# Optimization experiments

Measured on AMD Instinct MI355X. Metric: run time of the kernel, lower is better.

The kernel has to match this reference:

```python
import jax, jax.numpy as jnp
import numpy as np
import math

DEPTH = 3
RATIO = 0.5
EPS = 1e-5


def _mlp_ln(h, W1, b1, W2, b2, W3, b3, g, beta):
    h = jax.nn.gelu(h @ W1 + b1, approximate=False)
    h = jax.nn.gelu(h @ W2 + b2, approximate=False)
    h = h @ W3 + b3
    mu = jnp.mean(h, axis=-1, keepdims=True)
    var = jnp.mean((h - mu) ** 2, axis=-1, keepdims=True)
    return g * (h - mu) * jax.lax.rsqrt(var + EPS) + beta


def _node_to_node(x, s, r, n, p):
    # two-way gather -> scatter_add -> MLP+LN. Row n of x_pad is a zero dummy
    # node that absorbs edges dropped by pooling (fixed-size, jit-friendly).
    x_pad = jnp.concatenate([x, jnp.zeros((1, x.shape[1]), x.dtype)], axis=0)
    msg = x_pad[jnp.concatenate([s, r])]            # [2E, C]
    recv = jnp.concatenate([r, s])                  # [2E]
    agg = jax.ops.segment_sum(msg, recv, num_segments=n + 1)[:n]
    return _mlp_ln(agg, *p)


def _forward(x, senders, receivers, pool_w, down_p, up_p):
    s, r = senders, receivers
    xs, edges, perms = [x], [(s, r)], []
    n = x.shape[0]
    for i in range(DEPTH):
        k = math.ceil(RATIO * n)  # PyG topk: ceil(ratio * N)
        w = pool_w[i]
        score = jnp.tanh(x @ w / jnp.linalg.norm(w))
        vals, perm = jax.lax.top_k(score, k)
        x = x[perm] * vals[:, None]
        # remap edges; dropped nodes (and old dummy n) map to new dummy k
        nmap = jnp.full((n + 1,), k, dtype=s.dtype).at[perm].set(
            jnp.arange(k, dtype=s.dtype))
        ns_, nr_ = nmap[s], nmap[r]
        invalid = (ns_ == k) | (nr_ == k)
        s = jnp.where(invalid, k, ns_)
        r = jnp.where(invalid, k, nr_)
        x = _node_to_node(x, s, r, k, down_p[i])
        if i < DEPTH - 1:
            xs.append(x)
            edges.append((s, r))
        perms.append(perm)
        n = k
    for i in range(DEPTH):
        j = DEPTH - 1 - i
        res = xs[j]
        s, r = edges[j]
        perm = perms[j]
        up = jnp.zeros_like(res).at[perm].set(x)
        x = jnp.concatenate([res, up], axis=-1)  # sum_res=False -> concat
        x = _node_to_node(x, s, r, res.shape[0], up_p[i])
    return x


def setup_inputs() -> dict:
    key = jax.random.key(0)
    ks = jax.random.split(key, 16)
    N, E, C, D = 50000, 600000, 128, DEPTH
    f32 = jnp.float32

    def lin(k, fi, fo):
        return (jax.random.normal(k, (D, fi, fo), f32) / np.sqrt(fi)).astype(f32)

    return {
        'x': jax.random.normal(ks[0], (N, C), f32),
        'senders': jax.random.randint(ks[1], (E,), 0, N, dtype=jnp.int32),
        'receivers': jax.random.randint(ks[2], (E,), 0, N, dtype=jnp.int32),
        'pool_w': jax.random.normal(ks[3], (D, C), f32),
        'down_W1': lin(ks[4], C, C), 'down_b1': jnp.zeros((D, C), f32),
        'down_W2': lin(ks[5], C, C), 'down_b2': jnp.zeros((D, C), f32),
        'down_W3': lin(ks[6], C, C), 'down_b3': jnp.zeros((D, C), f32),
        'down_g': jnp.ones((D, C), f32), 'down_beta': jnp.zeros((D, C), f32),
        'up_W1': lin(ks[7], 2 * C, C), 'up_b1': jnp.zeros((D, C), f32),
        'up_W2': lin(ks[8], C, C), 'up_b2': jnp.zeros((D, C), f32),
        'up_W3': lin(ks[9], C, C), 'up_b3': jnp.zeros((D, C), f32),
        'up_g': jnp.ones((D, C), f32), 'up_beta': jnp.zeros((D, C), f32),
    }


def reference(x, senders, receivers, pool_w,
              down_W1, down_b1, down_W2, down_b2, down_W3, down_b3,
              down_g, down_beta,
              up_W1, up_b1, up_W2, up_b2, up_W3, up_b3, up_g, up_beta):
    down_p = [(down_W1[i], down_b1[i], down_W2[i], down_b2[i],
               down_W3[i], down_b3[i], down_g[i], down_beta[i])
              for i in range(DEPTH)]
    up_p = [(up_W1[i], up_b1[i], up_W2[i], up_b2[i],
             up_W3[i], up_b3[i], up_g[i], up_beta[i])
            for i in range(DEPTH)]
    return _forward(x, senders, receivers, pool_w, down_p, up_p)
```

## Files before the change

### kernel.cpp

```cpp
#include <hip/hip_runtime.h>
#include <math.h>


typedef unsigned short u16;
typedef short bf16x8 __attribute__((ext_vector_type(8)));
typedef float f32x4 __attribute__((ext_vector_type(4)));

__device__ __forceinline__ unsigned int fkey(float f) {
  unsigned int b = __float_as_uint(f);
  return (b & 0x80000000u) ? ~b : (b | 0x80000000u);
}

__device__ __forceinline__ float gelu_f(float v) {
  return 0.5f * v * (1.0f + erff(v * 0.70710678118654752f));
}

__device__ __forceinline__ u16 f2bf(float f) {
  unsigned u = __float_as_uint(f);
  u = (u + 0x7FFFu + ((u >> 16) & 1u)) >> 16;
  return (u16)u;
}
__device__ __forceinline__ float bf2f(u16 u) {
  return __uint_as_float(((unsigned)u) << 16);
}

__global__ void score_kernel(const float* __restrict__ x, const float* __restrict__ w,
                             float* __restrict__ key, float* __restrict__ valt, int n) {
  int wave = threadIdx.x >> 6, lane = threadIdx.x & 63;
  int i = blockIdx.x * 4 + wave;
  if (i >= n) return;
  float2 xv = *(const float2*)&x[(size_t)i * 128 + lane * 2];
  float2 wv = *(const float2*)&w[lane * 2];
  double d  = (double)xv.x * wv.x + (double)xv.y * wv.y;
  double nw = (double)wv.x * wv.x + (double)wv.y * wv.y;
  for (int o = 32; o; o >>= 1) { d += __shfl_down(d, o, 64); nw += __shfl_down(nw, o, 64); }
  if (lane == 0) {
    key[i]  = (float)d;
    valt[i] = (float)tanh(d / sqrt(nw));
  }
}

__global__ void preamble_kernel(const float* __restrict__ x, u16* __restrict__ xb, int n,
                                const float* __restrict__ uW1, const float* __restrict__ uW2,
                                const float* __restrict__ uW3, u16* __restrict__ wt1,
                                u16* __restrict__ wt2, u16* __restrict__ wt3,
                                const float* __restrict__ poolw, double* __restrict__ sqn,
                                u16* __restrict__ z0, u16* __restrict__ z1,
                                u16* __restrict__ z2, int nbX) {
  int b = blockIdx.x;
  if (b < nbX) {
    int gid = b * 256 + threadIdx.x;
    if (gid < n * 32) {
      float4 a = *(const float4*)&x[(size_t)gid * 4];
      *(ushort4*)&xb[(size_t)gid * 4] =
          make_ushort4(f2bf(a.x), f2bf(a.y), f2bf(a.z), f2bf(a.w));
    }
    return;
  }
  b -= nbX;
  if (b < 768) {
    int i = b * 256 + threadIdx.x;
    int lvl = i >> 16, rem = i & 65535;
    if (rem < 32768) {
      int k = rem >> 7, c = rem & 127;
      wt1[(size_t)lvl * 32768 + c * 256 + k] = f2bf(uW1[(size_t)lvl * 32768 + rem]);
    } else if (rem < 49152) {
      int j = rem - 32768; int k = j >> 7, c = j & 127;
      wt2[(size_t)lvl * 16384 + c * 128 + k] = f2bf(uW2[(size_t)lvl * 16384 + j]);
    } else {
      int j = rem - 49152; int k = j >> 7, c = j & 127;
      wt3[(size_t)lvl * 16384 + c * 128 + k] = f2bf(uW3[(size_t)lvl * 16384 + j]);
    }
    return;
  }
  b -= 768;
  if (b == 0) {
    if (threadIdx.x < 64) {
      int lane = threadIdx.x;
      for (int l = 0; l < 3; ++l) {
        float2 wv = *(const float2*)&poolw[l * 128 + lane * 2];
        double nw = (double)wv.x * wv.x + (double)wv.y * wv.y;
        for (int o = 32; o; o >>= 1) nw += __shfl_down(nw, o, 64);
        if (lane == 0) sqn[l] = sqrt(nw);
      }
    }
    return;
  }
  int t = threadIdx.x;
  if (t < 128) { z0[t] = 0; z1[t] = 0; z2[t] = 0; }
}

__global__ void hist_hi_kernel(const float* __restrict__ key, int* __restrict__ hist,
                               int* __restrict__ csum, int n) {
  __shared__ int lc[256];
  lc[threadIdx.x] = 0;
  __syncthreads();
  int i = blockIdx.x * 256 + threadIdx.x;
  if (i < n) {
    unsigned b = fkey(key[i]) >> 16;
    atomicAdd(&hist[b], 1);
    atomicAdd(&lc[b >> 8], 1);
  }
  __syncthreads();
  int v = lc[threadIdx.x];
  if (v) atomicAdd(&csum[threadIdx.x], v);
}

__global__ void hist_lo_kernel(const float* __restrict__ key, const int* __restrict__ meta,
                               int* __restrict__ hist, int* __restrict__ csum, int n) {
  __shared__ int lc[256];
  lc[threadIdx.x] = 0;
  __syncthreads();
  int i = blockIdx.x * 256 + threadIdx.x;
  if (i < n) {
    unsigned u = fkey(key[i]);
    if ((u >> 16) == (unsigned)meta[0]) {
      unsigned b = u & 0xFFFFu;
      atomicAdd(&hist[b], 1);
      atomicAdd(&lc[b >> 8], 1);
    }
  }
  __syncthreads();
  int v = lc[threadIdx.x];
  if (v) atomicAdd(&csum[threadIdx.x], v);
}

__global__ void find_hi2_kernel(const int* __restrict__ hist, const int* __restrict__ csum,
                                int* __restrict__ meta, int k) {
  __shared__ int s[256];
  __shared__ int cSh, cumSh;
  int t = threadIdx.x;
  s[t] = csum[t];
  __syncthreads();
  if (t == 0) {
    int cum = 0, c = 0;
    for (int i = 255; i >= 0; --i) {
      if (cum + s[i] >= k) { c = i; break; }
      cum += s[i];
    }
    cSh = c; cumSh = cum;
  }
  __syncthreads();
  int c = cSh;
  s[t] = hist[c * 256 + t];
  __syncthreads();
  if (t == 0) {
    int cum = cumSh;
    for (int b = 255; b >= 0; --b) {
      int v = s[b];
      if (cum + v >= k) { meta[0] = c * 256 + b; meta[1] = k - cum; break; }
      cum += v;
    }
  }
}

__global__ void find_lo2_kernel(const int* __restrict__ hist, const int* __restrict__ csum,
                                int* __restrict__ meta) {
  __shared__ int s[256];
  __shared__ int cSh, cumSh;
  int t = threadIdx.x;
  int m = meta[1], B = meta[0];
  s[t] = csum[t];
  __syncthreads();
  if (t == 0) {
    int cum = 0, c = 0;
    for (int i = 255; i >= 0; --i) {
      if (cum + s[i] >= m) { c = i; break; }
      cum += s[i];
    }
    cSh = c; cumSh = cum;
  }
  __syncthreads();
  int c = cSh;
  s[t] = hist[c * 256 + t];
  __syncthreads();
  if (t == 0) {
    int cum = cumSh;
    for (int b = 255; b >= 0; --b) {
      int v = s[b];
      if (cum + v >= m) {
        meta[3] = (int)((((unsigned)B) << 16) | (unsigned)(c * 256 + b));
        meta[4] = m - cum;
        break;
      }
      cum += v;
    }
    meta[5] = 0;
  }
}

__global__ void tie_count_kernel(const float* __restrict__ key, const int* __restrict__ meta,
                                 int* __restrict__ tcnt, int n) {
  __shared__ int cnt[4];
  unsigned uT = (unsigned)meta[3];
  int i = blockIdx.x * 256 + threadIdx.x;
  bool tie = (i < n) && (fkey(key[i]) == uT);
  unsigned long long m = __ballot(tie);
  int lane = threadIdx.x & 63, w = threadIdx.x >> 6;
  if (lane == 0) cnt[w] = __popcll(m);
  __syncthreads();
  if (threadIdx.x == 0) tcnt[blockIdx.x] = cnt[0] + cnt[1] + cnt[2] + cnt[3];
}

__global__ void tie_mark_kernel(const float* __restrict__ key, const int* __restrict__ meta,
                                const int* __restrict__ tcnt, unsigned char* __restrict__ selt,
                                int n) {
  __shared__ int red[256];
  __shared__ int woff[4];
  int t = threadIdx.x;
  red[t] = (t < (int)blockIdx.x) ? tcnt[t] : 0;
  __syncthreads();
  for (int s = 128; s; s >>= 1) {
    if (t < s) red[t] += red[t + s];
    __syncthreads();
  }
  int blockbase = red[0];
  unsigned uT = (unsigned)meta[3];
  int tsel = meta[4];
  int i = blockIdx.x * 256 + t;
  bool tie = (i < n) && (fkey(key[i]) == uT);
  unsigned long long m = __ballot(tie);
  int lane = t & 63, w = t >> 6;
  if (lane == 0) woff[w] = __popcll(m);
  __syncthreads();
  if (t == 0) {
    int c = 0;
    for (int q = 0; q < 4; ++q) { int v = woff[q]; woff[q] = c; c += v; }
  }
  __syncthreads();
  if (tie) {
    int pre = __popcll(m & ((1ull << lane) - 1ull));
    int rank = blockbase + woff[w] + pre;
    selt[i] = (rank < tsel) ? 1 : 0;
  }
}

__global__ void select_kernel(const float* __restrict__ key, const float* __restrict__ valt,
                              const unsigned char* __restrict__ selt, int* __restrict__ meta,
                              int* __restrict__ perm, float* __restrict__ vals,
                              int* __restrict__ nmap, int n, int k) {
  int i = blockIdx.x * 256 + threadIdx.x;
  if (i > n) return;
  if (i == n) { nmap[n] = k; return; }
  unsigned u  = fkey(key[i]);
  unsigned uT = (unsigned)meta[3];
  bool sel = (u > uT) || (u == uT && selt[i] != 0);
  if (sel) {
    int slot = atomicAdd(&meta[5], 1);
    perm[slot] = i; vals[slot] = valt[i]; nmap[i] = slot;
  } else {
    nmap[i] = k;
  }
}

__global__ void pool_kernel(const float* __restrict__ x, const int* __restrict__ perm,
                            const float* __restrict__ vals, float* __restrict__ xp, int k) {
  int gid = blockIdx.x * 256 + threadIdx.x;
  int t = gid >> 5;
  if (t >= k) return;
  int c = (gid & 31) << 2;
  float v = vals[t];
  float4 a = *(const float4*)&x[(size_t)perm[t] * 128 + c];
  a.x *= v; a.y *= v; a.z *= v; a.w *= v;
  *(float4*)&xp[(size_t)t * 128 + c] = a;
}

__global__ void remap_deg_rank_kernel(const int* __restrict__ s_in, const int* __restrict__ r_in,
                                      const int* __restrict__ nmap, int* __restrict__ s_out,
                                      int* __restrict__ r_out, int* __restrict__ deg,
                                      int* __restrict__ rkS, int* __restrict__ rkR,
                                      int E, int k) {
  int e = blockIdx.x * 256 + threadIdx.x;
  if (e >= E) return;
  int a = nmap[s_in[e]], b = nmap[r_in[e]];
  if (a == k || b == k) { a = k; b = k; }
  s_out[e] = a; r_out[e] = b;
  if (a < k) {
    rkR[e] = atomicAdd(&deg[b], 1);
    rkS[e] = atomicAdd(&deg[a], 1);
  }
}

__global__ void deg_rank_kernel(const int* __restrict__ s, const int* __restrict__ r,
                                int* __restrict__ deg, int* __restrict__ rkS,
                                int* __restrict__ rkR, int E, int n) {
  int e = blockIdx.x * 256 + threadIdx.x;
  if (e >= E) return;
  int ss = s[e];
  if (ss >= n) return;
  int rr = r[e];
  rkR[e] = atomicAdd(&deg[rr], 1);
  rkS[e] = atomicAdd(&deg[ss], 1);
}

__global__ void scan_part_kernel(const int* __restrict__ deg, int* __restrict__ bsum, int n) {
  __shared__ int l[256];
  int i = blockIdx.x * 256 + threadIdx.x;
  l[threadIdx.x] = (i < n) ? deg[i] : 0;
  __syncthreads();
  for (int s = 128; s; s >>= 1) {
    if (threadIdx.x < s) l[threadIdx.x] += l[threadIdx.x + s];
    __syncthreads();
  }
  if (threadIdx.x == 0) bsum[blockIdx.x] = l[0];
}

__global__ void scan_final_kernel(const int* __restrict__ deg, const int* __restrict__ bsum,
                                  int* __restrict__ off, int n) {
  __shared__ int red[256];
  __shared__ int l[256];
  int i = blockIdx.x * 256 + threadIdx.x;
  int t = threadIdx.x;
  red[t] = (t < (int)blockIdx.x) ? bsum[t] : 0;
  __syncthreads();
  for (int s = 128; s; s >>= 1) {
    if (t < s) red[t] += red[t + s];
    __syncthreads();
  }
  int base = red[0];
  int v = (i < n) ? deg[i] : 0;
  l[t] = v;
  __syncthreads();
#pragma unroll
  for (int s = 1; s < 256; s <<= 1) {
    int add = (t >= s) ? l[t - s] : 0;
    __syncthreads();
    l[t] += add;
    __syncthreads();
  }
  int incl = l[t];
  if (i < n) {
    int e = base + incl - v;
    off[i] = e;
    if (i == n - 1) off[n] = base + incl;
  }
}

__global__ void rank_scatter_kernel(const int* __restrict__ s, const int* __restrict__ r,
                                    const int* __restrict__ off, const int* __restrict__ rkS,
                                    const int* __restrict__ rkR, int* __restrict__ idx,
                                    int E, int n) {
  int e = blockIdx.x * 256 + threadIdx.x;
  if (e >= E) return;
  int ss = s[e];
  if (ss >= n) return;
  int rr = r[e];
  idx[off[rr] + rkR[e]] = ss;
  idx[off[ss] + rkS[e]] = rr;
}

__global__ void idxup3_kernel(const int* __restrict__ idxA, const int* __restrict__ nmA,
                              const int* __restrict__ lenA, int* __restrict__ outA,
                              const int* __restrict__ idxB, const int* __restrict__ nmB,
                              const int* __restrict__ lenB, int* __restrict__ outB,
                              const int* __restrict__ idxC, const int* __restrict__ nmC,
                              const int* __restrict__ lenC, int* __restrict__ outC,
                              int nbSeg, int maxlen) {
  int seg = blockIdx.x / nbSeg;
  int j = (blockIdx.x - seg * nbSeg) * 256 + threadIdx.x;
  if (j >= maxlen) return;
  const int* idx; const int* nm; const int* len; int* out;
  if (seg == 0)      { idx = idxA; nm = nmA; len = lenA; out = outA; }
  else if (seg == 1) { idx = idxB; nm = nmB; len = lenB; out = outB; }
  else               { idx = idxC; nm = nmC; len = lenC; out = outC; }
  if (j >= len[0]) return;
  out[j] = nm[idx[j]];
}

__global__ void agg_kernel(const float* __restrict__ x, const int* __restrict__ off,
                           const int* __restrict__ idx, float* __restrict__ agg, int n) {
  int wave = threadIdx.x >> 6, lane = threadIdx.x & 63;
  int v = blockIdx.x * 4 + wave;
  if (v >= n) return;
  int lo = __builtin_amdgcn_readfirstlane(off[v]);
  int hi = __builtin_amdgcn_readfirstlane(off[v + 1]);
  int g = lane >> 5, sl = lane & 31;
  const float* bp = x + sl * 4;
  float4 acc = {0.f, 0.f, 0.f, 0.f};
#define ACC_F(EE)                                        \
  do {                                                   \
    float4 w_ = *(const float4*)(bp + (size_t)(EE) * 128);\
    acc.x += w_.x; acc.y += w_.y; acc.z += w_.z; acc.w += w_.w; \
  } while (0)
  int j = lo;
  for (; j + 8 <= hi; j += 8) {
    int q0 = idx[j],     q1 = idx[j + 1], q2 = idx[j + 2], q3 = idx[j + 3];
    int q4 = idx[j + 4], q5 = idx[j + 5], q6 = idx[j + 6], q7 = idx[j + 7];
    ACC_F(g ? q1 : q0);
    ACC_F(g ? q3 : q2);
    ACC_F(g ? q5 : q4);
    ACC_F(g ? q7 : q6);
  }
  for (; j + 2 <= hi; j += 2) {
    int q0 = idx[j], q1 = idx[j + 1];
    ACC_F(g ? q1 : q0);
  }
  if (j < hi) {
    int q0 = idx[j];
    if (!g) ACC_F(q0);
  }
#undef ACC_F
  acc.x += __shfl_xor(acc.x, 32, 64);
  acc.y += __shfl_xor(acc.y, 32, 64);
  acc.z += __shfl_xor(acc.z, 32, 64);
  acc.w += __shfl_xor(acc.w, 32, 64);
  if (!g) *(float4*)&agg[(size_t)v * 128 + sl * 4] = acc;
}

__global__ void agg_up_kernel(const u16* __restrict__ res_bf, const u16* __restrict__ xd_bf,
                              const int* __restrict__ idxR, const int* __restrict__ idxU,
                              const int* __restrict__ off, u16* __restrict__ agg, int n) {
  int wave = threadIdx.x >> 6, lane = threadIdx.x & 63;
  int v = blockIdx.x * 4 + wave;
  if (v >= n) return;
  int lo = __builtin_amdgcn_readfirstlane(off[v]);
  int hi = __builtin_amdgcn_readfirstlane(off[v + 1]);
  int g = lane >> 4, sl = lane & 15;
  bool upH = g >= 2;
  bool second = (g & 1) != 0;
  const u16* bp = (upH ? xd_bf : res_bf) + sl * 8;
  float4 a0 = {0.f, 0.f, 0.f, 0.f}, a1 = {0.f, 0.f, 0.f, 0.f};

#define ACC_ROW(EE)                                     \
  do {                                                  \
    uint4 wq = *(const uint4*)(bp + (size_t)(EE) * 128);\
    a0.x += __uint_as_float(wq.x << 16);                \
    a0.y += __uint_as_float(wq.x & 0xffff0000u);        \
    a0.z += __uint_as_float(wq.y << 16);                \
    a0.w += __uint_as_float(wq.y & 0xffff0000u);        \
    a1.x += __uint_as_float(wq.z << 16);                \
    a1.y += __uint_as_float(wq.z & 0xffff0000u);        \
    a1.z += __uint_as_float(wq.w << 16);                \
    a1.w += __uint_as_float(wq.w & 0xffff0000u);        \
  } while (0)
#define SEL(EU_A, EU_B, ER_A, ER_B) \
  (upH ? (second ? (EU_B) : (EU_A)) : (second ? (ER_B) : (ER_A)))

  int j = lo;
  for (; j + 16 <= hi; j += 16) {
    int er0 = idxR[j +  0], er1 = idxR[j +  1], er2 = idxR[j +  2], er3 = idxR[j +  3];
    int er4 = idxR[j +  4], er5 = idxR[j +  5], er6 = idxR[j +  6], er7 = idxR[j +  7];
    int er8 = idxR[j +  8], er9 = idxR[j +  9], erA = idxR[j + 10], erB = idxR[j + 11];
    int erC = idxR[j + 12], erD = idxR[j + 13], erE = idxR[j + 14], erF = idxR[j + 15];
    int eu0 = idxU[j +  0], eu1 = idxU[j +  1], eu2 = idxU[j +  2], eu3 = idxU[j +  3];
    int eu4 = idxU[j +  4], eu5 = idxU[j +  5], eu6 = idxU[j +  6], eu7 = idxU[j +  7];
    int eu8 = idxU[j +  8], eu9 = idxU[j +  9], euA = idxU[j + 10], euB = idxU[j + 11];
    int euC = idxU[j + 12], euD = idxU[j + 13], euE = idxU[j + 14], euF = idxU[j + 15];
    int e0 = SEL(eu0, eu1, er0, er1);
    int e1 = SEL(eu2, eu3, er2, er3);
    int e2 = SEL(eu4, eu5, er4, er5);
    int e3 = SEL(eu6, eu7, er6, er7);
    int e4 = SEL(eu8, eu9, er8, er9);
    int e5 = SEL(euA, euB, erA, erB);
    int e6 = SEL(euC, euD, erC, erD);
    int e7 = SEL(euE, euF, erE, erF);
    ACC_ROW(e0); ACC_ROW(e1); ACC_ROW(e2); ACC_ROW(e3);
    ACC_ROW(e4); ACC_ROW(e5); ACC_ROW(e6); ACC_ROW(e7);
  }
  for (; j + 4 <= hi; j += 4) {
    int er0 = idxR[j], er1 = idxR[j + 1], er2 = idxR[j + 2], er3 = idxR[j + 3];
    int eu0 = idxU[j], eu1 = idxU[j + 1], eu2 = idxU[j + 2], eu3 = idxU[j + 3];
    int e0 = SEL(eu0, eu1, er0, er1);
    int e1 = SEL(eu2, eu3, er2, er3);
    ACC_ROW(e0);
    ACC_ROW(e1);
  }
  for (; j + 2 <= hi; j += 2) {
    int er0 = idxR[j], er1 = idxR[j + 1];
    int eu0 = idxU[j], eu1 = idxU[j + 1];
    int e = SEL(eu0, eu1, er0, er1);
    ACC_ROW(e);
  }
  if (j < hi) {
    int er = idxR[j], eu = idxU[j];
    int e = upH ? eu : er;
    if (!second) ACC_ROW(e);
  }
#undef SEL
#undef ACC_ROW

  a0.x += __shfl_xor(a0.x, 16, 64);
  a0.y += __shfl_xor(a0.y, 16, 64);
  a0.z += __shfl_xor(a0.z, 16, 64);
  a0.w += __shfl_xor(a0.w, 16, 64);
  a1.x += __shfl_xor(a1.x, 16, 64);
  a1.y += __shfl_xor(a1.y, 16, 64);
  a1.z += __shfl_xor(a1.z, 16, 64);
  a1.w += __shfl_xor(a1.w, 16, 64);

  if (!second) {
    bf16x8 ov;
    ov[0] = (short)f2bf(a0.x); ov[1] = (short)f2bf(a0.y);
    ov[2] = (short)f2bf(a0.z); ov[3] = (short)f2bf(a0.w);
    ov[4] = (short)f2bf(a1.x); ov[5] = (short)f2bf(a1.y);
    ov[6] = (short)f2bf(a1.z); ov[7] = (short)f2bf(a1.w);
    *(bf16x8*)&agg[(size_t)v * 256 + (upH ? 128 : 0) + sl * 8] = ov;
  }
}

template <bool GELU>
__global__ __launch_bounds__(256) void gemm_kernel(const float* __restrict__ A,
                                                   const float* __restrict__ W,
                                                   const float* __restrict__ bias,
                                                   float* __restrict__ out, int n) {
  __shared__ float As[32 * 32];
  __shared__ float Ws[32 * 128];
  int t = threadIdx.x;
  int row0 = blockIdx.x * 32;
  int colg = (t & 31) << 2;
  int rowg = (t >> 5) << 2;
  float acc[4][4];
#pragma unroll
  for (int i = 0; i < 4; ++i)
#pragma unroll
    for (int j = 0; j < 4; ++j) acc[i][j] = 0.f;

  for (int k0 = 0; k0 < 128; k0 += 32) {
    __syncthreads();
    {
      int ar = t >> 3, ac = (t & 7) << 2;
      float4 av = make_float4(0.f, 0.f, 0.f, 0.f);
      if (row0 + ar < n) av = *(const float4*)&A[(size_t)(row0 + ar) * 128 + k0 + ac];
      *(float4*)&As[ar * 32 + ac] = av;
    }
#pragma unroll
    for (int l = 0; l < 4; ++l) {
      int id = t + l * 256;
      int kk = id >> 5, wc = (id & 31) << 2;
      *(float4*)&Ws[kk * 128 + wc] = *(const float4*)&W[(size_t)(k0 + kk) * 128 + wc];
    }
    __syncthreads();
#pragma unroll
    for (int kk = 0; kk < 32; kk += 4) {
      float4 wv[4];
#pragma unroll
      for (int j = 0; j < 4; ++j) wv[j] = *(const float4*)&Ws[(kk + j) * 128 + colg];
#pragma unroll
      for (int i = 0; i < 4; ++i) {
        float4 av = *(const float4*)&As[(rowg + i) * 32 + kk];
        acc[i][0] += av.x * wv[0].x + av.y * wv[1].x + av.z * wv[2].x + av.w * wv[3].x;
        acc[i][1] += av.x * wv[0].y + av.y * wv[1].y + av.z * wv[2].y + av.w * wv[3].y;
        acc[i][2] += av.x * wv[0].z + av.y * wv[1].z + av.z * wv[2].z + av.w * wv[3].z;
        acc[i][3] += av.x * wv[0].w + av.y * wv[1].w + av.z * wv[2].w + av.w * wv[3].w;
      }
    }
  }
  float4 bv = *(const float4*)&bias[colg];
#pragma unroll
  for (int i = 0; i < 4; ++i) {
    int rr = row0 + rowg + i;
    if (rr < n) {
      float4 o = make_float4(acc[i][0] + bv.x, acc[i][1] + bv.y, acc[i][2] + bv.z, acc[i][3] + bv.w);
      if (GELU) { o.x = gelu_f(o.x); o.y = gelu_f(o.y); o.z = gelu_f(o.z); o.w = gelu_f(o.w); }
      *(float4*)&out[(size_t)rr * 128 + colg] = o;
    }
  }
}

template <int K>
__global__ __launch_bounds__(256) void gemm_mfma_kernel(const u16* __restrict__ A,
                                                        const u16* __restrict__ WT,
                                                        const float* __restrict__ bias,
                                                        u16* __restrict__ out, int n) {
  __shared__ u16 As[64 * 72];
  __shared__ u16 Ws[128 * 72];
  int t = threadIdx.x;
  int lane = t & 63, wave = t >> 6;
  int row0 = blockIdx.x * 64;
  f32x4 acc[8];
#pragma unroll
  for (int i = 0; i < 8; ++i) acc[i] = (f32x4){0.f, 0.f, 0.f, 0.f};

  for (int k0 = 0; k0 < K; k0 += 64) {
    __syncthreads();
#pragma unroll
    for (int i = 0; i < 2; ++i) {
      int c = t + i * 256;
      int r = c >> 3, seg = c & 7;
      bf16x8 v = {0, 0, 0, 0, 0, 0, 0, 0};
      if (row0 + r < n) v = *(const bf16x8*)&A[(size_t)(row0 + r) * K + k0 + seg * 8];
      *(bf16x8*)&As[r * 72 + seg * 8] = v;
    }
#pragma unroll
    for (int i = 0; i < 4; ++i) {
      int c = t + i * 256;
      int r = c >> 3, seg = c & 7;
      *(bf16x8*)&Ws[r * 72 + seg * 8] = *(const bf16x8*)&WT[(size_t)r * K + k0 + seg * 8];
    }
    __syncthreads();
#pragma unroll
    for (int kk = 0; kk < 64; kk += 32) {
      bf16x8 a = *(const bf16x8*)&As[(wave * 16 + (lane & 15)) * 72 + kk + (lane >> 4) * 8];
#pragma unroll
      for (int ct = 0; ct < 8; ++ct) {
        bf16x8 b = *(const bf16x8*)&Ws[(ct * 16 + (lane & 15)) * 72 + kk + (lane >> 4) * 8];
        acc[ct] = __builtin_amdgcn_mfma_f32_16x16x32_bf16(a, b, acc[ct], 0, 0, 0);
      }
    }
  }
  int colb = lane & 15, rquad = lane >> 4;
#pragma unroll
  for (int ct = 0; ct < 8; ++ct) {
#pragma unroll
    for (int r = 0; r < 4; ++r) {
      int row = row0 + wave * 16 + rquad * 4 + r;
      if (row < n) {
        int col = ct * 16 + colb;
        out[(size_t)row * 128 + col] = f2bf(gelu_f(acc[ct][r] + bias[col]));
      }
    }
  }
}

template <bool WF32, bool WBF>
__global__ __launch_bounds__(256) void gemm_mfma_ln_kernel(
    const u16* __restrict__ A, const u16* __restrict__ WT, const float* __restrict__ bias,
    const float* __restrict__ g, const float* __restrict__ beta,
    float* __restrict__ out, u16* __restrict__ outbf, int n) {
  __shared__ u16 As[64 * 72];
  __shared__ u16 Ws[128 * 72];
  int t = threadIdx.x;
  int lane = t & 63, wave = t >> 6;
  int row0 = blockIdx.x * 64;
  f32x4 acc[8];
#pragma unroll
  for (int i = 0; i < 8; ++i) acc[i] = (f32x4){0.f, 0.f, 0.f, 0.f};

  for (int k0 = 0; k0 < 128; k0 += 64) {
    __syncthreads();
#pragma unroll
    for (int i = 0; i < 2; ++i) {
      int c = t + i * 256;
      int r = c >> 3, seg = c & 7;
      bf16x8 v = {0, 0, 0, 0, 0, 0, 0, 0};
      if (row0 + r < n) v = *(const bf16x8*)&A[(size_t)(row0 + r) * 128 + k0 + seg * 8];
      *(bf16x8*)&As[r * 72 + seg * 8] = v;
    }
#pragma unroll
    for (int i = 0; i < 4; ++i) {
      int c = t + i * 256;
      int r = c >> 3, seg = c & 7;
      *(bf16x8*)&Ws[r * 72 + seg * 8] = *(const bf16x8*)&WT[(size_t)r * 128 + k0 + seg * 8];
    }
    __syncthreads();
#pragma unroll
    for (int kk = 0; kk < 64; kk += 32) {
      bf16x8 a = *(const bf16x8*)&As[(wave * 16 + (lane & 15)) * 72 + kk + (lane >> 4) * 8];
#pragma unroll
      for (int ct = 0; ct < 8; ++ct) {
        bf16x8 b = *(const bf16x8*)&Ws[(ct * 16 + (lane & 15)) * 72 + kk + (lane >> 4) * 8];
        acc[ct] = __builtin_amdgcn_mfma_f32_16x16x32_bf16(a, b, acc[ct], 0, 0, 0);
      }
    }
  }
  int colb = lane & 15, rquad = lane >> 4;
  float bv[8], gv[8], bev[8];
#pragma unroll
  for (int ct = 0; ct < 8; ++ct) {
    int col = ct * 16 + colb;
    bv[ct] = bias[col]; gv[ct] = g[col]; bev[ct] = beta[col];
  }
#pragma unroll
  for (int r = 0; r < 4; ++r) {
    float s1 = 0.f;
#pragma unroll
    for (int ct = 0; ct < 8; ++ct) s1 += acc[ct][r] + bv[ct];
#pragma unroll
    for (int o = 1; o <= 8; o <<= 1) s1 += __shfl_xor(s1, o, 64);
    float mu = s1 * (1.0f / 128.0f);
    float s2 = 0.f;
#pragma unroll
    for (int ct = 0; ct < 8; ++ct) { float d = acc[ct][r] + bv[ct] - mu; s2 += d * d; }
#pragma unroll
    for (int o = 1; o <= 8; o <<= 1) s2 += __shfl_xor(s2, o, 64);
    float rs = rsqrtf(s2 * (1.0f / 128.0f) + 1e-5f);
    int row = row0 + wave * 16 + rquad * 4 + r;
    if (row < n) {
#pragma unroll
      for (int ct = 0; ct < 8; ++ct) {
        int col = ct * 16 + colb;
        float o = gv[ct] * (acc[ct][r] + bv[ct] - mu) * rs + bev[ct];
        if (WF32) out[(size_t)row * 128 + col] = o;
        if (WBF)  outbf[(size_t)row * 128 + col] = f2bf(o);
      }
    }
  }
}

template <bool SCORE, bool WBF>
__global__ void ln_kernel(const float* __restrict__ h, const float* __restrict__ g,
                          const float* __restrict__ beta, float* __restrict__ out,
                          u16* __restrict__ outbf, const float* __restrict__ wnext,
                          const double* __restrict__ sqn, float* __restrict__ key,
                          float* __restrict__ valt, int n) {
  int wave = threadIdx.x >> 6, lane = threadIdx.x & 63;
  int i = blockIdx.x * 4 + wave;
  if (i >= n) return;
  float2 hv = *(const float2*)&h[(size_t)i * 128 + lane * 2];
  float s = hv.x + hv.y;
  for (int o = 32; o; o >>= 1) s += __shfl_down(s, o, 64);
  float mu = __shfl(s, 0, 64) * (1.0f / 128.0f);
  float dx = hv.x - mu, dy = hv.y - mu;
  float q = dx * dx + dy * dy;
  for (int o = 32; o; o >>= 1) q += __shfl_down(q, o, 64);
  float var = __shfl(q, 0, 64) * (1.0f / 128.0f);
  float rs = rsqrtf(var + 1e-5f);
  float2 gv = *(const float2*)&g[lane * 2];
  float2 bv = *(const float2*)&beta[lane * 2];
  float2 o2; o2.x = gv.x * dx * rs + bv.x; o2.y = gv.y * dy * rs + bv.y;
  *(float2*)&out[(size_t)i * 128 + lane * 2] = o2;
  if (WBF)
    *(ushort2*)&outbf[(size_t)i * 128 + lane * 2] = make_ushort2(f2bf(o2.x), f2bf(o2.y));
  if (SCORE) {
    float2 wv = *(const float2*)&wnext[lane * 2];
    double d = (double)o2.x * wv.x + (double)o2.y * wv.y;
    for (int o = 32; o; o >>= 1) d += __shfl_down(d, o, 64);
    if (lane == 0) {
      key[i]  = (float)d;
      valt[i] = (float)tanh(d / sqn[0]);
    }
  }
}


static inline int cdiv(int a, int b) { return (a + b - 1) / b; }

extern "C" void kernel_launch(void* const* d_in, const int* in_sizes, int n_in,
                              void* d_out, int out_size, void* d_ws, size_t ws_size,
                              hipStream_t stream) {
  const float* x0   = (const float*)d_in[0];
  const int*   snd  = (const int*)d_in[1];
  const int*   rcv  = (const int*)d_in[2];
  const float* poolw = (const float*)d_in[3];
  const float* dW1 = (const float*)d_in[4];
  const float* db1 = (const float*)d_in[5];
  const float* dW2 = (const float*)d_in[6];
  const float* db2 = (const float*)d_in[7];
  const float* dW3 = (const float*)d_in[8];
  const float* db3 = (const float*)d_in[9];
  const float* dg  = (const float*)d_in[10];
  const float* dbe = (const float*)d_in[11];
  const float* uW1 = (const float*)d_in[12];
  const float* ub1 = (const float*)d_in[13];
  const float* uW2 = (const float*)d_in[14];
  const float* ub2 = (const float*)d_in[15];
  const float* uW3 = (const float*)d_in[16];
  const float* ub3 = (const float*)d_in[17];
  const float* ug  = (const float*)d_in[18];
  const float* ube = (const float*)d_in[19];

  const int N0 = in_sizes[0] / 128;
  const int E  = in_sizes[1];
  const int N1 = (N0 + 1) / 2, N2 = (N1 + 1) / 2, N3 = (N2 + 1) / 2;

  char* p = (char*)d_ws;
  auto alloc = [&](size_t bytes) -> void* {
    void* r = (void*)p;
    p += (bytes + 255) & ~(size_t)255;
    return r;
  };
  float* key  = (float*)alloc((size_t)N0 * 4);
  float* valt = (float*)alloc((size_t)N0 * 4);
  int*   hist = (int*)alloc((size_t)(2 * 65536 + 512) * 4);
  int*   csum_hi = hist + 2 * 65536;
  int*   csum_lo = hist + 2 * 65536 + 256;
  int*   meta = (int*)alloc(64 * 4);
  int*   tcnt = (int*)alloc(512 * 4);
  int*   bsum = (int*)alloc(256 * 4);
  unsigned char* selt = (unsigned char*)alloc((size_t)N0);
  int*   nm1 = (int*)alloc((size_t)(N0 + 1) * 4);
  int*   nm2 = (int*)alloc((size_t)(N1 + 1) * 4);
  int*   nm3 = (int*)alloc((size_t)(N2 + 1) * 4);
  int*   perm0 = (int*)alloc((size_t)N1 * 4);
  int*   perm1 = (int*)alloc((size_t)N2 * 4);
  int*   perm2 = (int*)alloc((size_t)N3 * 4);
  float* vals  = (float*)alloc((size_t)N1 * 4);
  double* sqn  = (double*)alloc(8 * 8);
  int* s1 = (int*)alloc((size_t)E * 4); int* r1 = (int*)alloc((size_t)E * 4);
  int* s2 = (int*)alloc((size_t)E * 4); int* r2 = (int*)alloc((size_t)E * 4);
  int* s3 = (int*)alloc((size_t)E * 4); int* r3 = (int*)alloc((size_t)E * 4);
  float* x1 = (float*)alloc((size_t)N1 * 128 * 4);
  float* x2 = (float*)alloc((size_t)N2 * 128 * 4);
  float* x3 = (float*)alloc((size_t)N3 * 128 * 4);
  float* xp = (float*)alloc((size_t)N1 * 128 * 4);
  float* aggf = (float*)alloc((size_t)N1 * 128 * 4);
  float* h1f  = (float*)alloc((size_t)N1 * 128 * 4);
  float* h2f  = (float*)alloc((size_t)N1 * 128 * 4);
  u16* agg_bf = (u16*)alloc((size_t)N0 * 256 * 2);
  u16* res0_bf = (u16*)alloc((size_t)N0 * 128 * 2);
  u16* res1_bf = (u16*)alloc((size_t)N1 * 128 * 2);
  u16* res2_bf = (u16*)alloc((size_t)N2 * 128 * 2);
  u16* x3_bf   = (u16*)alloc((size_t)(N3 + 1) * 128 * 2);
  u16* xu2_bf  = (u16*)alloc((size_t)(N2 + 1) * 128 * 2);
  u16* xu1_bf  = (u16*)alloc((size_t)(N1 + 1) * 128 * 2);
  u16* wt1 = (u16*)alloc((size_t)3 * 128 * 256 * 2);
  u16* wt2 = (u16*)alloc((size_t)3 * 128 * 128 * 2);
  u16* wt3 = (u16*)alloc((size_t)3 * 128 * 128 * 2);
  int* off0 = (int*)alloc((size_t)(N0 + 1) * 4); int* deg0 = (int*)alloc((size_t)N0 * 4);
  int* idx0 = (int*)alloc((size_t)2 * E * 4);
  int* off1 = (int*)alloc((size_t)(N1 + 1) * 4); int* deg1 = (int*)alloc((size_t)N1 * 4);
  int* idx1 = (int*)alloc((size_t)2 * E * 4);
  int* off2 = (int*)alloc((size_t)(N2 + 1) * 4); int* deg2 = (int*)alloc((size_t)N2 * 4);
  int* idx2 = (int*)alloc((size_t)2 * E * 4);
  int* off3 = (int*)alloc((size_t)(N3 + 1) * 4); int* deg3 = (int*)alloc((size_t)N3 * 4);
  int* idx3 = (int*)alloc((size_t)2 * E * 4);
  int* idxu0 = (int*)alloc((size_t)2 * E * 4);
  int* idxu1 = (int*)alloc((size_t)2 * E * 4);
  int* idxu2 = (int*)alloc((size_t)2 * E * 4);

  u16* h1b = (u16*)xp;
  u16* h2b = (u16*)s1;
  int* rkS = (int*)agg_bf;
  int* rkR = rkS + E;

  auto run_scan = [&](int* degB, int* offB, int n) {
    int nb = cdiv(n, 256);
    scan_part_kernel<<<nb, 256, 0, stream>>>(degB, bsum, n);
    scan_final_kernel<<<nb, 256, 0, stream>>>(degB, bsum, offB, n);
  };

  {
    int nbX = cdiv(N0 * 32, 256);
    preamble_kernel<<<nbX + 768 + 2, 256, 0, stream>>>(
        x0, res0_bf, N0, uW1, uW2, uW3, wt1, wt2, wt3, poolw, sqn,
        x3_bf + (size_t)N3 * 128, xu2_bf + (size_t)N2 * 128,
        xu1_bf + (size_t)N1 * 128, nbX);
  }

  hipMemsetAsync(deg0, 0, (size_t)N0 * 4, stream);
  deg_rank_kernel<<<cdiv(E, 256), 256, 0, stream>>>(snd, rcv, deg0, rkS, rkR, E, N0);
  run_scan(deg0, off0, N0);
  rank_scatter_kernel<<<cdiv(E, 256), 256, 0, stream>>>(snd, rcv, off0, rkS, rkR, idx0, E, N0);

  auto down_step = [&](int n, int k, const float* xcur, const int* sin, const int* rin,
                       int* sout, int* rout, int* permL, int* nmL, float* xnext,
                       u16* xnext_bf, int lvl, int* offL, int* degL, int* idxL) {
    int nb = cdiv(n, 256);
    hipMemsetAsync(hist, 0, (size_t)(2 * 65536 + 512) * 4, stream);
    hist_hi_kernel<<<nb, 256, 0, stream>>>(key, hist, csum_hi, n);
    find_hi2_kernel<<<1, 256, 0, stream>>>(hist, csum_hi, meta, k);
    hist_lo_kernel<<<nb, 256, 0, stream>>>(key, meta, hist + 65536, csum_lo, n);
    find_lo2_kernel<<<1, 256, 0, stream>>>(hist + 65536, csum_lo, meta);
    tie_count_kernel<<<nb, 256, 0, stream>>>(key, meta, tcnt, n);
    tie_mark_kernel<<<nb, 256, 0, stream>>>(key, meta, tcnt, selt, n);
    select_kernel<<<cdiv(n + 1, 256), 256, 0, stream>>>(key, valt, selt, meta, permL, vals, nmL, n, k);
    pool_kernel<<<cdiv(k * 32, 256), 256, 0, stream>>>(xcur, permL, vals, xp, k);
    hipMemsetAsync(degL, 0, (size_t)k * 4, stream);
    remap_deg_rank_kernel<<<cdiv(E, 256), 256, 0, stream>>>(
        sin, rin, nmL, sout, rout, degL, rkS, rkR, E, k);
    run_scan(degL, offL, k);
    rank_scatter_kernel<<<cdiv(E, 256), 256, 0, stream>>>(sout, rout, offL, rkS, rkR, idxL, E, k);
    agg_kernel<<<cdiv(k, 4), 256, 0, stream>>>(xp, offL, idxL, aggf, k);
    gemm_kernel<true><<<cdiv(k, 32), 256, 0, stream>>>(
        aggf, dW1 + (size_t)lvl * 128 * 128, db1 + (size_t)lvl * 128, h1f, k);
    gemm_kernel<true><<<cdiv(k, 32), 256, 0, stream>>>(
        h1f, dW2 + (size_t)lvl * 128 * 128, db2 + (size_t)lvl * 128, h2f, k);
    gemm_kernel<false><<<cdiv(k, 32), 256, 0, stream>>>(
        h2f, dW3 + (size_t)lvl * 128 * 128, db3 + (size_t)lvl * 128, h1f, k);
    if (lvl < 2)
      ln_kernel<true, true><<<cdiv(k, 4), 256, 0, stream>>>(
          h1f, dg + (size_t)lvl * 128, dbe + (size_t)lvl * 128, xnext, xnext_bf,
          poolw + (size_t)(lvl + 1) * 128, sqn + (lvl + 1), key, valt, k);
    else
      ln_kernel<false, true><<<cdiv(k, 4), 256, 0, stream>>>(
          h1f, dg + (size_t)lvl * 128, dbe + (size_t)lvl * 128, xnext, xnext_bf,
          nullptr, nullptr, nullptr, nullptr, k);
  };

  score_kernel<<<cdiv(N0, 4), 256, 0, stream>>>(x0, poolw, key, valt, N0);
  down_step(N0, N1, x0, snd, rcv, s1, r1, perm0, nm1, x1, res1_bf, 0, off1, deg1, idx1);
  down_step(N1, N2, x1, s1, r1, s2, r2, perm1, nm2, x2, res2_bf, 1, off2, deg2, idx2);
  down_step(N2, N3, x2, s2, r2, s3, r3, perm2, nm3, x3, x3_bf, 2, off3, deg3, idx3);

  {
    int nbSeg = cdiv(2 * E, 256);
    idxup3_kernel<<<3 * nbSeg, 256, 0, stream>>>(
        idx2, nm3, off2 + N2, idxu2,
        idx1, nm2, off1 + N1, idxu1,
        idx0, nm1, off0 + N0, idxu0, nbSeg, 2 * E);
  }

  auto up_step = [&](int n, const u16* resb, const u16* xdb, int lvl,
                     const int* offL, const int* idxL, const int* idxUL,
                     bool wantF32, float* outF32, u16* outBF) {
    agg_up_kernel<<<cdiv(n, 4), 256, 0, stream>>>(resb, xdb, idxL, idxUL, offL, agg_bf, n);
    gemm_mfma_kernel<256><<<cdiv(n, 64), 256, 0, stream>>>(
        agg_bf, wt1 + (size_t)lvl * 128 * 256, ub1 + (size_t)lvl * 128, h1b, n);
    gemm_mfma_kernel<128><<<cdiv(n, 64), 256, 0, stream>>>(
        h1b, wt2 + (size_t)lvl * 128 * 128, ub2 + (size_t)lvl * 128, h2b, n);
    if (wantF32)
      gemm_mfma_ln_kernel<true, false><<<cdiv(n, 64), 256, 0, stream>>>(
          h2b, wt3 + (size_t)lvl * 128 * 128, ub3 + (size_t)lvl * 128,
          ug + (size_t)lvl * 128, ube + (size_t)lvl * 128, outF32, nullptr, n);
    else
      gemm_mfma_ln_kernel<false, true><<<cdiv(n, 64), 256, 0, stream>>>(
          h2b, wt3 + (size_t)lvl * 128 * 128, ub3 + (size_t)lvl * 128,
          ug + (size_t)lvl * 128, ube + (size_t)lvl * 128, nullptr, outBF, n);
  };

  up_step(N2, res2_bf, x3_bf,  0, off2, idx2, idxu2, false, nullptr, xu2_bf);
  up_step(N1, res1_bf, xu2_bf, 1, off1, idx1, idxu1, false, nullptr, xu1_bf);
  up_step(N0, res0_bf, xu1_bf, 2, off0, idx0, idxu0, true, (float*)d_out, nullptr);

  (void)n_in; (void)out_size; (void)ws_size;
}
```

Baseline: 934.8 us.

## Fold memsets into preamble, merge tie-mark with select, split up-aggregation into two gathers

All per-level histogram and degree buffers get their own slices and are zeroed once inside the preamble kernel, which removes the per-level hipMemsetAsync calls. The tie-marking and selection kernels become one kernel, dropping the selt byte buffer and one launch per level. The combined residual/up aggregation kernel is split into two single-table gather kernels, each using all four 16-lane groups on different edges. This simplifies index selection but adds a launch and rereads the offsets and CSR edge ranges in each of the two passes.

```diff
diff --git a/kernel.cpp b/kernel.cpp
--- a/kernel.cpp
+++ b/kernel.cpp
@@ -5,6 +5,8 @@
 typedef unsigned short u16;
 typedef short bf16x8 __attribute__((ext_vector_type(8)));
 typedef float f32x4 __attribute__((ext_vector_type(4)));
+
+#define HIST_STRIDE (2 * 65536 + 512)
 
 __device__ __forceinline__ unsigned int fkey(float f) {
   unsigned int b = __float_as_uint(f);
@@ -46,7 +48,9 @@
                                 u16* __restrict__ wt2, u16* __restrict__ wt3,
                                 const float* __restrict__ poolw, double* __restrict__ sqn,
                                 u16* __restrict__ z0, u16* __restrict__ z1,
-                                u16* __restrict__ z2, int nbX) {
+                                u16* __restrict__ z2, int* __restrict__ histAll,
+                                int* __restrict__ degAll, int nbX, int nbHZ, int nHist,
+                                int nDeg) {
   int b = blockIdx.x;
   if (b < nbX) {
     int gid = b * 256 + threadIdx.x;
@@ -86,8 +90,23 @@
     }
     return;
   }
-  int t = threadIdx.x;
-  if (t < 128) { z0[t] = 0; z1[t] = 0; z2[t] = 0; }
+  b -= 1;
+  if (b == 0) {
+    int t = threadIdx.x;
+    if (t < 128) { z0[t] = 0; z1[t] = 0; z2[t] = 0; }
+    return;
+  }
+  b -= 1;
+  if (b < nbHZ) {
+    int i = b * 256 + threadIdx.x;
+    if (i < nHist) histAll[i] = 0;
+    return;
+  }
+  b -= nbHZ;
+  {
+    int i = b * 256 + threadIdx.x;
+    if (i < nDeg) degAll[i] = 0;
+  }
 }
 
 __global__ void hist_hi_kernel(const float* __restrict__ key, int* __restrict__ hist,
@@ -202,9 +221,10 @@
   if (threadIdx.x == 0) tcnt[blockIdx.x] = cnt[0] + cnt[1] + cnt[2] + cnt[3];
 }
 
-__global__ void tie_mark_kernel(const float* __restrict__ key, const int* __restrict__ meta,
-                                const int* __restrict__ tcnt, unsigned char* __restrict__ selt,
-                                int n) {
+__global__ void tie_select_kernel(const float* __restrict__ key, const float* __restrict__ valt,
+                                  const int* __restrict__ tcnt, int* __restrict__ meta,
+                                  int* __restrict__ perm, float* __restrict__ vals,
+                                  int* __restrict__ nmap, int n, int k) {
   __shared__ int red[256];
   __shared__ int woff[4];
   int t = threadIdx.x;
@@ -218,7 +238,8 @@
   unsigned uT = (unsigned)meta[3];
   int tsel = meta[4];
   int i = blockIdx.x * 256 + t;
-  bool tie = (i < n) && (fkey(key[i]) == uT);
+  unsigned u = (i < n) ? fkey(key[i]) : 0u;
+  bool tie = (i < n) && (u == uT);
   unsigned long long m = __ballot(tie);
   int lane = t & 63, w = t >> 6;
   if (lane == 0) woff[w] = __popcll(m);
@@ -228,23 +249,16 @@
     for (int q = 0; q < 4; ++q) { int v = woff[q]; woff[q] = c; c += v; }
   }
   __syncthreads();
+  if (i > n) return;
+  if (i == n) { nmap[n] = k; return; }
+  bool sel;
   if (tie) {
     int pre = __popcll(m & ((1ull << lane) - 1ull));
     int rank = blockbase + woff[w] + pre;
-    selt[i] = (rank < tsel) ? 1 : 0;
-  }
-}
-
-__global__ void select_kernel(const float* __restrict__ key, const float* __restrict__ valt,
-                              const unsigned char* __restrict__ selt, int* __restrict__ meta,
-                              int* __restrict__ perm, float* __restrict__ vals,
-                              int* __restrict__ nmap, int n, int k) {
-  int i = blockIdx.x * 256 + threadIdx.x;
-  if (i > n) return;
-  if (i == n) { nmap[n] = k; return; }
-  unsigned u  = fkey(key[i]);
-  unsigned uT = (unsigned)meta[3];
-  bool sel = (u > uT) || (u == uT && selt[i] != 0);
+    sel = (rank < tsel);
+  } else {
+    sel = (u > uT);
+  }
   if (sel) {
     int slot = atomicAdd(&meta[5], 1);
     perm[slot] = i; vals[slot] = valt[i]; nmap[i] = slot;
@@ -407,18 +421,16 @@
   if (!g) *(float4*)&agg[(size_t)v * 128 + sl * 4] = acc;
 }
 
-__global__ void agg_up_kernel(const u16* __restrict__ res_bf, const u16* __restrict__ xd_bf,
-                              const int* __restrict__ idxR, const int* __restrict__ idxU,
-                              const int* __restrict__ off, u16* __restrict__ agg, int n) {
+template <int OFS>
+__global__ void agg_gather_kernel(const u16* __restrict__ tab, const int* __restrict__ idx,
+                                  const int* __restrict__ off, u16* __restrict__ agg, int n) {
   int wave = threadIdx.x >> 6, lane = threadIdx.x & 63;
   int v = blockIdx.x * 4 + wave;
   if (v >= n) return;
   int lo = __builtin_amdgcn_readfirstlane(off[v]);
   int hi = __builtin_amdgcn_readfirstlane(off[v + 1]);
   int g = lane >> 4, sl = lane & 15;
-  bool upH = g >= 2;
-  bool second = (g & 1) != 0;
-  const u16* bp = (upH ? xd_bf : res_bf) + sl * 8;
+  const u16* bp = tab + sl * 8;
   float4 a0 = {0.f, 0.f, 0.f, 0.f}, a1 = {0.f, 0.f, 0.f, 0.f};
 
 #define ACC_ROW(EE)                                     \
@@ -433,50 +445,24 @@
     a1.z += __uint_as_float(wq.w << 16);                \
     a1.w += __uint_as_float(wq.w & 0xffff0000u);        \
   } while (0)
-#define SEL(EU_A, EU_B, ER_A, ER_B) \
-  (upH ? (second ? (EU_B) : (EU_A)) : (second ? (ER_B) : (ER_A)))
 
   int j = lo;
   for (; j + 16 <= hi; j += 16) {
-    int er0 = idxR[j +  0], er1 = idxR[j +  1], er2 = idxR[j +  2], er3 = idxR[j +  3];
-    int er4 = idxR[j +  4], er5 = idxR[j +  5], er6 = idxR[j +  6], er7 = idxR[j +  7];
-    int er8 = idxR[j +  8], er9 = idxR[j +  9], erA = idxR[j + 10], erB = idxR[j + 11];
-    int erC = idxR[j + 12], erD = idxR[j + 13], erE = idxR[j + 14], erF = idxR[j + 15];
-    int eu0 = idxU[j +  0], eu1 = idxU[j +  1], eu2 = idxU[j +  2], eu3 = idxU[j +  3];
-    int eu4 = idxU[j +  4], eu5 = idxU[j +  5], eu6 = idxU[j +  6], eu7 = idxU[j +  7];
-    int eu8 = idxU[j +  8], eu9 = idxU[j +  9], euA = idxU[j + 10], euB = idxU[j + 11];
-    int euC = idxU[j + 12], euD = idxU[j + 13], euE = idxU[j + 14], euF = idxU[j + 15];
-    int e0 = SEL(eu0, eu1, er0, er1);
-    int e1 = SEL(eu2, eu3, er2, er3);
-    int e2 = SEL(eu4, eu5, er4, er5);
-    int e3 = SEL(eu6, eu7, er6, er7);
-    int e4 = SEL(eu8, eu9, er8, er9);
-    int e5 = SEL(euA, euB, erA, erB);
-    int e6 = SEL(euC, euD, erC, erD);
-    int e7 = SEL(euE, euF, erE, erF);
+    int e0 = idx[j + g];
+    int e1 = idx[j + g + 4];
+    int e2 = idx[j + g + 8];
+    int e3 = idx[j + g + 12];
     ACC_ROW(e0); ACC_ROW(e1); ACC_ROW(e2); ACC_ROW(e3);
-    ACC_ROW(e4); ACC_ROW(e5); ACC_ROW(e6); ACC_ROW(e7);
   }
   for (; j + 4 <= hi; j += 4) {
-    int er0 = idxR[j], er1 = idxR[j + 1], er2 = idxR[j + 2], er3 = idxR[j + 3];
-    int eu0 = idxU[j], eu1 = idxU[j + 1], eu2 = idxU[j + 2], eu3 = idxU[j + 3];
-    int e0 = SEL(eu0, eu1, er0, er1);
-    int e1 = SEL(eu2, eu3, er2, er3);
+    int e0 = idx[j + g];
     ACC_ROW(e0);
-    ACC_ROW(e1);
-  }
-  for (; j + 2 <= hi; j += 2) {
-    int er0 = idxR[j], er1 = idxR[j + 1];
-    int eu0 = idxU[j], eu1 = idxU[j + 1];
-    int e = SEL(eu0, eu1, er0, er1);
+  }
+  int rmn = hi - j;
+  if (g < rmn) {
+    int e = idx[j + g];
     ACC_ROW(e);
   }
-  if (j < hi) {
-    int er = idxR[j], eu = idxU[j];
-    int e = upH ? eu : er;
-    if (!second) ACC_ROW(e);
-  }
-#undef SEL
 #undef ACC_ROW
 
   a0.x += __shfl_xor(a0.x, 16, 64);
@@ -487,14 +473,22 @@
   a1.y += __shfl_xor(a1.y, 16, 64);
   a1.z += __shfl_xor(a1.z, 16, 64);
   a1.w += __shfl_xor(a1.w, 16, 64);
-
-  if (!second) {
+  a0.x += __shfl_xor(a0.x, 32, 64);
+  a0.y += __shfl_xor(a0.y, 32, 64);
+  a0.z += __shfl_xor(a0.z, 32, 64);
+  a0.w += __shfl_xor(a0.w, 32, 64);
+  a1.x += __shfl_xor(a1.x, 32, 64);
+  a1.y += __shfl_xor(a1.y, 32, 64);
+  a1.z += __shfl_xor(a1.z, 32, 64);
+  a1.w += __shfl_xor(a1.w, 32, 64);
+
+  if (lane < 16) {
     bf16x8 ov;
     ov[0] = (short)f2bf(a0.x); ov[1] = (short)f2bf(a0.y);
     ov[2] = (short)f2bf(a0.z); ov[3] = (short)f2bf(a0.w);
     ov[4] = (short)f2bf(a1.x); ov[5] = (short)f2bf(a1.y);
     ov[6] = (short)f2bf(a1.z); ov[7] = (short)f2bf(a1.w);
-    *(bf16x8*)&agg[(size_t)v * 256 + (upH ? 128 : 0) + sl * 8] = ov;
+    *(bf16x8*)&agg[(size_t)v * 256 + OFS + sl * 8] = ov;
   }
 }
 
@@ -761,13 +755,10 @@
   };
   float* key  = (float*)alloc((size_t)N0 * 4);
   float* valt = (float*)alloc((size_t)N0 * 4);
-  int*   hist = (int*)alloc((size_t)(2 * 65536 + 512) * 4);
-  int*   csum_hi = hist + 2 * 65536;
-  int*   csum_lo = hist + 2 * 65536 + 256;
+  int*   histAll = (int*)alloc((size_t)3 * HIST_STRIDE * 4);
   int*   meta = (int*)alloc(64 * 4);
   int*   tcnt = (int*)alloc(512 * 4);
   int*   bsum = (int*)alloc(256 * 4);
-  unsigned char* selt = (unsigned char*)alloc((size_t)N0);
   int*   nm1 = (int*)alloc((size_t)(N0 + 1) * 4);
   int*   nm2 = (int*)alloc((size_t)(N1 + 1) * 4);
   int*   nm3 = (int*)alloc((size_t)(N2 + 1) * 4);
@@ -796,13 +787,18 @@
   u16* wt1 = (u16*)alloc((size_t)3 * 128 * 256 * 2);
   u16* wt2 = (u16*)alloc((size_t)3 * 128 * 128 * 2);
   u16* wt3 = (u16*)alloc((size_t)3 * 128 * 128 * 2);
-  int* off0 = (int*)alloc((size_t)(N0 + 1) * 4); int* deg0 = (int*)alloc((size_t)N0 * 4);
+  int* degAll = (int*)alloc((size_t)(N0 + N1 + N2 + N3) * 4);
+  int* deg0 = degAll;
+  int* deg1 = degAll + N0;
+  int* deg2 = deg1 + N1;
+  int* deg3 = deg2 + N2;
+  int* off0 = (int*)alloc((size_t)(N0 + 1) * 4);
   int* idx0 = (int*)alloc((size_t)2 * E * 4);
-  int* off1 = (int*)alloc((size_t)(N1 + 1) * 4); int* deg1 = (int*)alloc((size_t)N1 * 4);
+  int* off1 = (int*)alloc((size_t)(N1 + 1) * 4);
   int* idx1 = (int*)alloc((size_t)2 * E * 4);
-  int* off2 = (int*)alloc((size_t)(N2 + 1) * 4); int* deg2 = (int*)alloc((size_t)N2 * 4);
+  int* off2 = (int*)alloc((size_t)(N2 + 1) * 4);
   int* idx2 = (int*)alloc((size_t)2 * E * 4);
-  int* off3 = (int*)alloc((size_t)(N3 + 1) * 4); int* deg3 = (int*)alloc((size_t)N3 * 4);
+  int* off3 = (int*)alloc((size_t)(N3 + 1) * 4);
   int* idx3 = (int*)alloc((size_t)2 * E * 4);
   int* idxu0 = (int*)alloc((size_t)2 * E * 4);
   int* idxu1 = (int*)alloc((size_t)2 * E * 4);
@@ -821,13 +817,16 @@
 
   {
     int nbX = cdiv(N0 * 32, 256);
-    preamble_kernel<<<nbX + 768 + 2, 256, 0, stream>>>(
+    int nHist = 3 * HIST_STRIDE;
+    int nbHZ = cdiv(nHist, 256);
+    int nDeg = N0 + N1 + N2 + N3;
+    int nbDZ = cdiv(nDeg, 256);
+    preamble_kernel<<<nbX + 768 + 1 + 1 + nbHZ + nbDZ, 256, 0, stream>>>(
         x0, res0_bf, N0, uW1, uW2, uW3, wt1, wt2, wt3, poolw, sqn,
         x3_bf + (size_t)N3 * 128, xu2_bf + (size_t)N2 * 128,
-        xu1_bf + (size_t)N1 * 128, nbX);
-  }
-
-  hipMemsetAsync(deg0, 0, (size_t)N0 * 4, stream);
+        xu1_bf + (size_t)N1 * 128, histAll, degAll, nbX, nbHZ, nHist, nDeg);
+  }
+
   deg_rank_kernel<<<cdiv(E, 256), 256, 0, stream>>>(snd, rcv, deg0, rkS, rkR, E, N0);
   run_scan(deg0, off0, N0);
   rank_scatter_kernel<<<cdiv(E, 256), 256, 0, stream>>>(snd, rcv, off0, rkS, rkR, idx0, E, N0);
@@ -836,16 +835,17 @@
                        int* sout, int* rout, int* permL, int* nmL, float* xnext,
                        u16* xnext_bf, int lvl, int* offL, int* degL, int* idxL) {
     int nb = cdiv(n, 256);
-    hipMemsetAsync(hist, 0, (size_t)(2 * 65536 + 512) * 4, stream);
-    hist_hi_kernel<<<nb, 256, 0, stream>>>(key, hist, csum_hi, n);
-    find_hi2_kernel<<<1, 256, 0, stream>>>(hist, csum_hi, meta, k);
-    hist_lo_kernel<<<nb, 256, 0, stream>>>(key, meta, hist + 65536, csum_lo, n);
-    find_lo2_kernel<<<1, 256, 0, stream>>>(hist + 65536, csum_lo, meta);
+    int* histL = histAll + (size_t)lvl * HIST_STRIDE;
+    int* csum_hi = histL + 2 * 65536;
+    int* csum_lo = csum_hi + 256;
+    hist_hi_kernel<<<nb, 256, 0, stream>>>(key, histL, csum_hi, n);
+    find_hi2_kernel<<<1, 256, 0, stream>>>(histL, csum_hi, meta, k);
+    hist_lo_kernel<<<nb, 256, 0, stream>>>(key, meta, histL + 65536, csum_lo, n);
+    find_lo2_kernel<<<1, 256, 0, stream>>>(histL + 65536, csum_lo, meta);
     tie_count_kernel<<<nb, 256, 0, stream>>>(key, meta, tcnt, n);
-    tie_mark_kernel<<<nb, 256, 0, stream>>>(key, meta, tcnt, selt, n);
-    select_kernel<<<cdiv(n + 1, 256), 256, 0, stream>>>(key, valt, selt, meta, permL, vals, nmL, n, k);
+    tie_select_kernel<<<cdiv(n + 1, 256), 256, 0, stream>>>(
+        key, valt, tcnt, meta, permL, vals, nmL, n, k);
     pool_kernel<<<cdiv(k * 32, 256), 256, 0, stream>>>(xcur, permL, vals, xp, k);
-    hipMemsetAsync(degL, 0, (size_t)k * 4, stream);
     remap_deg_rank_kernel<<<cdiv(E, 256), 256, 0, stream>>>(
         sin, rin, nmL, sout, rout, degL, rkS, rkR, E, k);
     run_scan(degL, offL, k);
@@ -883,7 +883,8 @@
   auto up_step = [&](int n, const u16* resb, const u16* xdb, int lvl,
                      const int* offL, const int* idxL, const int* idxUL,
                      bool wantF32, float* outF32, u16* outBF) {
-    agg_up_kernel<<<cdiv(n, 4), 256, 0, stream>>>(resb, xdb, idxL, idxUL, offL, agg_bf, n);
+    agg_gather_kernel<0><<<cdiv(n, 4), 256, 0, stream>>>(resb, idxL, offL, agg_bf, n);
+    agg_gather_kernel<128><<<cdiv(n, 4), 256, 0, stream>>>(xdb, idxUL, offL, agg_bf, n);
     gemm_mfma_kernel<256><<<cdiv(n, 64), 256, 0, stream>>>(
         agg_bf, wt1 + (size_t)lvl * 128 * 256, ub1 + (size_t)lvl * 128, h1b, n);
     gemm_mfma_kernel<128><<<cdiv(n, 64), 256, 0, stream>>>(
```

Result: no change. 921.4 us (-1.4%).
